# Optimization experiments

Hardware: AMD Instinct MI355X
Metric: run time of the kernel (lower is better)

## Reference

```python
import jax, jax.numpy as jnp
import numpy as np

NUM_HEADS = 16
EPS = 1e-5  # torch nn.LayerNorm default


def _ln(x, g, b):
    m = jnp.mean(x, axis=-1, keepdims=True)
    v = jnp.var(x, axis=-1, keepdims=True)
    return (x - m) / jnp.sqrt(v + EPS) * g + b


def _attn(q, k, v, proj_w, proj_b):
    B, N, C = q.shape
    S = k.shape[1]
    H = NUM_HEADS
    D = C // H
    qh = q.reshape(B, N, H, D).transpose(0, 2, 1, 3)
    kh = k.reshape(B, S, H, D).transpose(0, 2, 1, 3)
    vh = v.reshape(B, S, H, D).transpose(0, 2, 1, 3)
    scores = jnp.einsum('bhnd,bhsd->bhns', qh, kh) * (D ** -0.5)
    aw = jax.nn.softmax(scores, axis=-1)
    o = jnp.einsum('bhns,bhsd->bhnd', aw, vh)
    o = o.transpose(0, 2, 1, 3).reshape(B, N, C)
    return o @ proj_w + proj_b


def _mlp(x, w1, b1, w2, b2):
    h = jax.nn.gelu(x @ w1 + b1, approximate=False)  # torch nn.GELU (exact erf)
    return h @ w2 + b2


def setup_inputs() -> dict:
    key = jax.random.key(0)
    ks = jax.random.split(key, 12)
    B, N, C = 4, 512, 1024
    H = 4 * C
    s = 0.02
    return {
        'x': jax.random.normal(ks[0], (B, N, C), jnp.float32),
        'y': jax.random.normal(ks[1], (B, N, C), jnp.float32),
        'norm1_g': jnp.ones((C,), jnp.float32),
        'norm1_b': jnp.zeros((C,), jnp.float32),
        'norm2_g': jnp.ones((C,), jnp.float32),
        'norm2_b': jnp.zeros((C,), jnp.float32),
        'proj_w': jax.random.normal(ks[2], (C, C), jnp.float32) * s,
        'proj_b': jnp.zeros((C,), jnp.float32),
        'fc1_w': jax.random.normal(ks[3], (C, H), jnp.float32) * s,
        'fc1_b': jnp.zeros((H,), jnp.float32),
        'fc2_w': jax.random.normal(ks[4], (H, C), jnp.float32) * s,
        'fc2_b': jnp.zeros((C,), jnp.float32),
        'is_selfatt': 1,
    }


def reference(x, y, norm1_g, norm1_b, norm2_g, norm2_b, proj_w, proj_b,
              fc1_w, fc1_b, fc2_w, fc2_b, is_selfatt):
    for _ in range(4):
        if is_selfatt:
            xn = _ln(x, norm1_g, norm1_b)
            x = x + _attn(xn, xn, xn, proj_w, proj_b)
            x = x + _mlp(_ln(x, norm2_g, norm2_b), fc1_w, fc1_b, fc2_w, fc2_b)
            yn = _ln(y, norm1_g, norm1_b)
            y = y + _attn(yn, yn, yn, proj_w, proj_b)
            y = y + _mlp(_ln(y, norm2_g, norm2_b), fc1_w, fc1_b, fc2_w, fc2_b)
        xn = _ln(x, norm1_g, norm1_b)
        yn = _ln(y, norm1_g, norm1_b)
        x1 = x + _attn(xn, yn, yn, proj_w, proj_b)
        x1 = x1 + _mlp(_ln(x1, norm2_g, norm2_b), fc1_w, fc1_b, fc2_w, fc2_b)
        y1 = y + _attn(yn, xn, xn, proj_w, proj_b)
        y1 = y1 + _mlp(_ln(y1, norm2_g, norm2_b), fc1_w, fc1_b, fc2_w, fc2_b)
    return (x1, y1)
```

## Files before the change

kernel.cpp:

```cpp
#include <hip/hip_runtime.h>
#include <hip/hip_bf16.h>
#include <math.h>

#define BDIM 4
#define SEQ 512
#define CH 1024
#define NH 16
#define HD 64
#define HIDN 4096
#define ROWS (BDIM * SEQ)
#define MROWS (2 * ROWS)
#define BHTOT (BDIM * NH)

using bf16 = __hip_bfloat16;
typedef __attribute__((ext_vector_type(4))) float f32x4;
typedef __attribute__((ext_vector_type(8))) short bf16x8;

typedef __attribute__((address_space(1))) const unsigned int GU32;
typedef __attribute__((address_space(3))) unsigned int LU32;

__device__ __forceinline__ void gload16(const bf16* g, bf16* l) {
  __builtin_amdgcn_global_load_lds((GU32*)g, (LU32*)l, 16, 0, 0);
}

__global__ __launch_bounds__(256) void ln_bf16_kernel(
    const float* __restrict__ x, const float* __restrict__ g,
    const float* __restrict__ b, bf16* __restrict__ out) {
  int row = blockIdx.x;
  int t = threadIdx.x;
  const float4 v = reinterpret_cast<const float4*>(x + (size_t)row * CH)[t];
  float s = v.x + v.y + v.z + v.w;
  float s2 = v.x * v.x + v.y * v.y + v.z * v.z + v.w * v.w;
#pragma unroll
  for (int o = 32; o > 0; o >>= 1) {
    s += __shfl_down(s, o);
    s2 += __shfl_down(s2, o);
  }
  __shared__ float red[10];
  int lane = t & 63, wid = t >> 6;
  if (lane == 0) { red[wid] = s; red[4 + wid] = s2; }
  __syncthreads();
  if (t == 0) {
    float ts = red[0] + red[1] + red[2] + red[3];
    float ts2 = red[4] + red[5] + red[6] + red[7];
    float mean = ts * (1.0f / CH);
    float var = ts2 * (1.0f / CH) - mean * mean;
    red[8] = mean;
    red[9] = rsqrtf(var + 1e-5f);
  }
  __syncthreads();
  float mean = red[8], rstd = red[9];
  const float4 gv = reinterpret_cast<const float4*>(g)[t];
  const float4 bv = reinterpret_cast<const float4*>(b)[t];
  alignas(8) bf16 o4[4];
  o4[0] = __float2bfloat16((v.x - mean) * rstd * gv.x + bv.x);
  o4[1] = __float2bfloat16((v.y - mean) * rstd * gv.y + bv.y);
  o4[2] = __float2bfloat16((v.z - mean) * rstd * gv.z + bv.z);
  o4[3] = __float2bfloat16((v.w - mean) * rstd * gv.w + bv.w);
  reinterpret_cast<uint2*>(out + (size_t)row * CH)[t] = *reinterpret_cast<const uint2*>(o4);
}

__global__ __launch_bounds__(256) void head_transpose_kernel(
    const bf16* __restrict__ src, bf16* __restrict__ dst) {
  __shared__ bf16 t[32][33];
  int bh = blockIdx.z, b = bh >> 4, h = bh & 15;
  int s0 = blockIdx.x * 32, d0 = blockIdx.y * 32;
  int tx = threadIdx.x & 31, ty = threadIdx.x >> 5;
  const bf16* sp = src + ((size_t)(b * SEQ + s0)) * CH + h * HD + d0;
  for (int i = ty; i < 32; i += 8) t[i][tx] = sp[(size_t)i * CH + tx];
  __syncthreads();
  bf16* dp = dst + ((size_t)bh * HD + d0) * SEQ + s0;
  for (int i = ty; i < 32; i += 8) dp[(size_t)i * SEQ + tx] = t[tx][i];
}

__global__ __launch_bounds__(256) void wt_transpose_kernel(
    const float* __restrict__ W, bf16* __restrict__ WT, int K, int Nout) {
  __shared__ float t[32][33];
  int k0 = blockIdx.x * 32, n0 = blockIdx.y * 32;
  int tx = threadIdx.x & 31, ty = threadIdx.x >> 5;
  for (int i = ty; i < 32; i += 8)
    t[i][tx] = W[(size_t)(k0 + i) * Nout + n0 + tx];
  __syncthreads();
  for (int i = ty; i < 32; i += 8)
    WT[(size_t)(n0 + i) * K + k0 + tx] = __float2bfloat16(t[tx][i]);
}

template <int MODE>
__global__ __launch_bounds__(256) void gemm128(
    const bf16* __restrict__ A, int lda,
    const bf16* __restrict__ Bt, int ldb,
    void* __restrict__ Cout, int ldc,
    const float* __restrict__ base, const float* __restrict__ bias,
    int K) {
  int m0 = blockIdx.x * 128, n0 = blockIdx.y * 128;
  __shared__ bf16 As[3][128 * 32];
  __shared__ bf16 Bs[3][128 * 32];
  int tid = threadIdx.x, wid = tid >> 6, lane = tid & 63;
  int wr = wid >> 1, wc = wid & 1;
  int srow = tid >> 2;
  int scol = (tid & 3) << 3;
  const bf16* ga = &A[(size_t)(m0 + srow) * lda + scol];
  const bf16* gb = &Bt[(size_t)(n0 + srow) * ldb + scol];
  int fr = lane & 15, kr = lane >> 4;
  f32x4 acc[4][4] = {};

  auto stage = [&](int b, int k0) {
    gload16(ga + k0, As[b] + tid * 8);
    gload16(ga + (size_t)64 * lda + k0, As[b] + 2048 + tid * 8);
    gload16(gb + k0, Bs[b] + tid * 8);
    gload16(gb + (size_t)64 * ldb + k0, Bs[b] + 2048 + tid * 8);
  };
  auto compute = [&](int b) {
    bf16x8 aF[4], bF[4];
#pragma unroll
    for (int m = 0; m < 4; ++m)
      aF[m] = *reinterpret_cast<const bf16x8*>(&As[b][(wr * 64 + m * 16 + fr) * 32 + kr * 8]);
#pragma unroll
    for (int n = 0; n < 4; ++n)
      bF[n] = *reinterpret_cast<const bf16x8*>(&Bs[b][(wc * 64 + n * 16 + fr) * 32 + kr * 8]);
#pragma unroll
    for (int m = 0; m < 4; ++m)
#pragma unroll
      for (int n = 0; n < 4; ++n)
        acc[m][n] = __builtin_amdgcn_mfma_f32_16x16x32_bf16(aF[m], bF[n], acc[m][n], 0, 0, 0);
  };

  int nt = K / 32;
  stage(0, 0);
  stage(1, 32);
  for (int t = 0; t < nt - 2; ++t) {
    stage((t + 2) % 3, (t + 2) * 32);
    asm volatile("s_waitcnt vmcnt(8)" ::: "memory");
    __builtin_amdgcn_s_barrier();
    __builtin_amdgcn_sched_barrier(0);
    compute(t % 3);
    __builtin_amdgcn_s_barrier();
  }
  asm volatile("s_waitcnt vmcnt(4)" ::: "memory");
  __builtin_amdgcn_s_barrier();
  __builtin_amdgcn_sched_barrier(0);
  compute((nt - 2) % 3);
  asm volatile("s_waitcnt vmcnt(0)" ::: "memory");
  __builtin_amdgcn_s_barrier();
  __builtin_amdgcn_sched_barrier(0);
  compute((nt - 1) % 3);

  int colL = lane & 15;
  int rbase = (lane >> 4) * 4;
#pragma unroll
  for (int n = 0; n < 4; ++n) {
    int gc = n0 + wc * 64 + n * 16 + colL;
    float bv = bias ? bias[gc] : 0.0f;
#pragma unroll
    for (int m = 0; m < 4; ++m)
#pragma unroll
      for (int j = 0; j < 4; ++j) {
        int gr = m0 + wr * 64 + m * 16 + rbase + j;
        float v = acc[m][n][j] + bv;
        size_t idx = (size_t)gr * ldc + gc;
        if (MODE == 0) {
          ((float*)Cout)[idx] = base[idx] + v;
        } else {
          float gl = 0.5f * v * (1.0f + erff(v * 0.70710678118654752f));
          ((bf16*)Cout)[idx] = __float2bfloat16(gl);
        }
      }
  }
}

__global__ __launch_bounds__(512) void attn_fused(
    const bf16* __restrict__ ln1, const bf16* __restrict__ vT,
    bf16* __restrict__ out, int xorb) {
  __shared__ bf16 kv[3][64 * 64];
  __shared__ bf16 Pl[128 * 512];
  int bh = blockIdx.y;
  int b = bh >> 4, h = bh & 15;
  int kvb = b ^ xorb;
  int kvbh = kvb * NH + h;
  int m0 = blockIdx.x * 128;
  int tid = threadIdx.x, wid = tid >> 6, lane = tid & 63;
  int fr = lane & 15, kr = lane >> 4;
  int srow = tid >> 3;
  int scol8 = ((tid & 7) ^ (srow & 7)) << 3;
  const bf16* kbase = ln1 + ((size_t)(kvb * SEQ + srow)) * CH + h * HD + scol8;
  const bf16* vbase = vT + ((size_t)kvbh * HD + srow) * SEQ + scol8;

  int qrow = m0 + wid * 16 + fr;
  const bf16* qbase = ln1 + ((size_t)(b * SEQ) + qrow) * CH + h * HD;
  bf16x8 qF0 = *reinterpret_cast<const bf16x8*>(qbase + kr * 8);
  bf16x8 qF1 = *reinterpret_cast<const bf16x8*>(qbase + 32 + kr * 8);

  f32x4 acc[32];
#pragma unroll
  for (int n = 0; n < 32; ++n) acc[n] = (f32x4){0.f, 0.f, 0.f, 0.f};

  gload16(kbase, kv[0] + tid * 8);
  gload16(kbase + (size_t)64 * CH, kv[1] + tid * 8);
#pragma unroll
  for (int c = 0; c < 8; ++c) {
    if (c + 2 < 8) gload16(kbase + (size_t)(c + 2) * 64 * CH, kv[(c + 2) % 3] + tid * 8);
    if (c + 2 < 8)      asm volatile("s_waitcnt vmcnt(2)" ::: "memory");
    else if (c + 1 < 8) asm volatile("s_waitcnt vmcnt(1)" ::: "memory");
    else                asm volatile("s_waitcnt vmcnt(0)" ::: "memory");
    __builtin_amdgcn_s_barrier();
    __builtin_amdgcn_sched_barrier(0);
    const char* kb = (const char*)kv[c % 3];
#pragma unroll
    for (int nf = 0; nf < 4; ++nf) {
      int sl = nf * 16 + fr;
      int byt = sl * 128 + kr * 16;
      bf16x8 k0 = *reinterpret_cast<const bf16x8*>(kb + (byt ^ ((sl & 7) << 4)));
      bf16x8 k1 = *reinterpret_cast<const bf16x8*>(kb + ((byt + 64) ^ ((sl & 7) << 4)));
      acc[c * 4 + nf] = __builtin_amdgcn_mfma_f32_16x16x32_bf16(qF0, k0, acc[c * 4 + nf], 0, 0, 0);
      acc[c * 4 + nf] = __builtin_amdgcn_mfma_f32_16x16x32_bf16(qF1, k1, acc[c * 4 + nf], 0, 0, 0);
    }
    __builtin_amdgcn_s_barrier();
  }

  float mx[4], sum[4], inv[4];
#pragma unroll
  for (int j = 0; j < 4; ++j) {
    float m = acc[0][j];
#pragma unroll
    for (int n = 1; n < 32; ++n) m = fmaxf(m, acc[n][j]);
    m = fmaxf(m, __shfl_xor(m, 1));
    m = fmaxf(m, __shfl_xor(m, 2));
    m = fmaxf(m, __shfl_xor(m, 4));
    m = fmaxf(m, __shfl_xor(m, 8));
    mx[j] = m * 0.125f;
  }
#pragma unroll
  for (int j = 0; j < 4; ++j) sum[j] = 0.f;
#pragma unroll
  for (int n = 0; n < 32; ++n)
#pragma unroll
    for (int j = 0; j < 4; ++j) {
      float p = exp2f((acc[n][j] * 0.125f - mx[j]) * 1.4426950408889634f);
      acc[n][j] = p;
      sum[j] += p;
    }
#pragma unroll
  for (int j = 0; j < 4; ++j) {
    float s = sum[j];
    s += __shfl_xor(s, 1);
    s += __shfl_xor(s, 2);
    s += __shfl_xor(s, 4);
    s += __shfl_xor(s, 8);
    inv[j] = 1.0f / s;
  }
  {
    char* pb = (char*)Pl;
#pragma unroll
    for (int n = 0; n < 32; ++n)
#pragma unroll
      for (int j = 0; j < 4; ++j) {
        int pr = wid * 16 + (lane >> 4) * 4 + j;
        int pc = fr + 16 * n;
        int byt = (pr * 1024 + pc * 2) ^ ((pr & 7) << 4);
        *reinterpret_cast<bf16*>(pb + byt) = __float2bfloat16(acc[n][j]);
      }
  }

  f32x4 oacc[4] = {};
  int prow = wid * 16 + fr;
  gload16(vbase, kv[0] + tid * 8);
  gload16(vbase + 64, kv[1] + tid * 8);
#pragma unroll
  for (int c = 0; c < 8; ++c) {
    if (c + 2 < 8) gload16(vbase + (size_t)(c + 2) * 64, kv[(c + 2) % 3] + tid * 8);
    if (c + 2 < 8)      asm volatile("s_waitcnt vmcnt(2)" ::: "memory");
    else if (c + 1 < 8) asm volatile("s_waitcnt vmcnt(1)" ::: "memory");
    else                asm volatile("s_waitcnt vmcnt(0)" ::: "memory");
    __builtin_amdgcn_s_barrier();
    __builtin_amdgcn_sched_barrier(0);
    const char* vb = (const char*)kv[c % 3];
    const char* pb = (const char*)Pl;
#pragma unroll
    for (int ks = 0; ks < 2; ++ks) {
      int pby = (prow * 1024 + (c * 64 + ks * 32 + kr * 8) * 2) ^ ((prow & 7) << 4);
      bf16x8 pF = *reinterpret_cast<const bf16x8*>(pb + pby);
#pragma unroll
      for (int nf = 0; nf < 4; ++nf) {
        int dl = nf * 16 + fr;
        int vby = (dl * 128 + ks * 64 + kr * 16) ^ ((dl & 7) << 4);
        bf16x8 vF = *reinterpret_cast<const bf16x8*>(vb + vby);
        oacc[nf] = __builtin_amdgcn_mfma_f32_16x16x32_bf16(pF, vF, oacc[nf], 0, 0, 0);
      }
    }
    __builtin_amdgcn_s_barrier();
  }

#pragma unroll
  for (int nf = 0; nf < 4; ++nf)
#pragma unroll
    for (int j = 0; j < 4; ++j) {
      int r = m0 + wid * 16 + (lane >> 4) * 4 + j;
      int d = fr + 16 * nf;
      out[((size_t)(b * SEQ) + r) * CH + h * HD + d] = __float2bfloat16(oacc[nf][j] * inv[j]);
    }
}

extern "C" void kernel_launch(void* const* d_in, const int* in_sizes, int n_in,
                              void* d_out, int out_size, void* d_ws, size_t ws_size,
                              hipStream_t stream) {
  const float* x_in  = (const float*)d_in[0];
  const float* y_in  = (const float*)d_in[1];
  const float* n1g   = (const float*)d_in[2];
  const float* n1b   = (const float*)d_in[3];
  const float* n2g   = (const float*)d_in[4];
  const float* n2b   = (const float*)d_in[5];
  const float* projw = (const float*)d_in[6];
  const float* projb = (const float*)d_in[7];
  const float* fc1w  = (const float*)d_in[8];
  const float* fc1b  = (const float*)d_in[9];
  const float* fc2w  = (const float*)d_in[10];
  const float* fc2b  = (const float*)d_in[11];

  char* p = (char*)d_ws;
  auto alloc = [&](size_t bytes) {
    char* r = p;
    p += (bytes + 255) & ~(size_t)255;
    return r;
  };
  float* xybuf  = (float*)alloc((size_t)MROWS * CH * 4);
  float* x1y1   = (float*)alloc((size_t)MROWS * CH * 4);
  bf16*  ln1out = (bf16*)alloc((size_t)MROWS * CH * 2);
  bf16*  ln2out = (bf16*)alloc((size_t)MROWS * CH * 2);
  bf16*  vTall  = (bf16*)alloc((size_t)2 * BHTOT * HD * SEQ * 2);
  bf16*  attnout= (bf16*)alloc((size_t)MROWS * CH * 2);
  bf16*  hbuf   = (bf16*)alloc((size_t)MROWS * HIDN * 2);
  bf16*  projWT = (bf16*)alloc((size_t)CH * CH * 2);
  bf16*  fc1WT  = (bf16*)alloc((size_t)HIDN * CH * 2);
  bf16*  fc2WT  = (bf16*)alloc((size_t)CH * HIDN * 2);
  if ((size_t)(p - (char*)d_ws) > ws_size) return;

  float* outxy = (float*)d_out;

  hipMemcpyAsync(xybuf, x_in, (size_t)ROWS * CH * 4, hipMemcpyDeviceToDevice, stream);
  hipMemcpyAsync(xybuf + (size_t)ROWS * CH, y_in, (size_t)ROWS * CH * 4,
                 hipMemcpyDeviceToDevice, stream);

  wt_transpose_kernel<<<dim3(CH / 32, CH / 32), 256, 0, stream>>>(projw, projWT, CH, CH);
  wt_transpose_kernel<<<dim3(CH / 32, HIDN / 32), 256, 0, stream>>>(fc1w, fc1WT, CH, HIDN);
  wt_transpose_kernel<<<dim3(HIDN / 32, CH / 32), 256, 0, stream>>>(fc2w, fc2WT, HIDN, CH);

  auto attn_all = [&](int xorb) {
    attn_fused<<<dim3(SEQ / 128, 2 * BHTOT), 512, 0, stream>>>(ln1out, vTall, attnout, xorb);
  };
  auto proj_merged = [&](const float* rbase, float* dst) {
    gemm128<0><<<dim3(MROWS / 128, CH / 128), 256, 0, stream>>>(
        attnout, CH, projWT, CH, dst, CH, rbase, projb, CH);
  };
  auto mlp_merged = [&](const float* bsrc, float* dst) {
    ln_bf16_kernel<<<MROWS, 256, 0, stream>>>(bsrc, n2g, n2b, ln2out);
    gemm128<3><<<dim3(MROWS / 128, HIDN / 128), 256, 0, stream>>>(
        ln2out, CH, fc1WT, CH, hbuf, HIDN, nullptr, fc1b, CH);
    gemm128<0><<<dim3(MROWS / 128, CH / 128), 256, 0, stream>>>(
        hbuf, HIDN, fc2WT, HIDN, dst, CH, bsrc, fc2b, HIDN);
  };

  for (int it = 0; it < 4; ++it) {
    ln_bf16_kernel<<<MROWS, 256, 0, stream>>>(xybuf, n1g, n1b, ln1out);
    head_transpose_kernel<<<dim3(SEQ / 32, HD / 32, 2 * BHTOT), 256, 0, stream>>>(ln1out, vTall);
    attn_all(0);
    proj_merged(xybuf, xybuf);
    mlp_merged(xybuf, xybuf);
  }
  ln_bf16_kernel<<<MROWS, 256, 0, stream>>>(xybuf, n1g, n1b, ln1out);
  head_transpose_kernel<<<dim3(SEQ / 32, HD / 32, 2 * BHTOT), 256, 0, stream>>>(ln1out, vTall);
  attn_all(4);
  proj_merged(xybuf, x1y1);
  mlp_merged(x1y1, outxy);
}
```

Baseline: 1.169 ms.

## Swizzle GEMM LDS layout and parameterize pipeline ring depth

XOR-swizzles the 16-byte column chunks within each LDS row of the A/B tiles, so that MFMA fragment reads from different rows hit different banks. This aims to cut LDS bank conflicts. The software pipeline is generalized to a templated ring depth, with the N=1024 GEMMs using 4 stages to hide more global latency and fc1 keeping 3. The deeper ring uses more LDS per block, which may reduce occupancy, and the drain waitcnt logic is hand-coded per ring depth.

```diff
diff --git a/kernel.cpp b/kernel.cpp
--- a/kernel.cpp
+++ b/kernel.cpp
@@ -85,7 +85,7 @@
     WT[(size_t)(n0 + i) * K + k0 + tx] = __float2bfloat16(t[tx][i]);
 }
 
-template <int MODE>
+template <int MODE, int RING>
 __global__ __launch_bounds__(256) void gemm128(
     const bf16* __restrict__ A, int lda,
     const bf16* __restrict__ Bt, int ldb,
@@ -93,12 +93,12 @@
     const float* __restrict__ base, const float* __restrict__ bias,
     int K) {
   int m0 = blockIdx.x * 128, n0 = blockIdx.y * 128;
-  __shared__ bf16 As[3][128 * 32];
-  __shared__ bf16 Bs[3][128 * 32];
+  __shared__ bf16 As[RING][128 * 32];
+  __shared__ bf16 Bs[RING][128 * 32];
   int tid = threadIdx.x, wid = tid >> 6, lane = tid & 63;
   int wr = wid >> 1, wc = wid & 1;
   int srow = tid >> 2;
-  int scol = (tid & 3) << 3;
+  int scol = ((tid & 3) ^ (srow & 3)) << 3;
   const bf16* ga = &A[(size_t)(m0 + srow) * lda + scol];
   const bf16* gb = &Bt[(size_t)(n0 + srow) * ldb + scol];
   int fr = lane & 15, kr = lane >> 4;
@@ -113,11 +113,15 @@
   auto compute = [&](int b) {
     bf16x8 aF[4], bF[4];
 #pragma unroll
-    for (int m = 0; m < 4; ++m)
-      aF[m] = *reinterpret_cast<const bf16x8*>(&As[b][(wr * 64 + m * 16 + fr) * 32 + kr * 8]);
-#pragma unroll
-    for (int n = 0; n < 4; ++n)
-      bF[n] = *reinterpret_cast<const bf16x8*>(&Bs[b][(wc * 64 + n * 16 + fr) * 32 + kr * 8]);
+    for (int m = 0; m < 4; ++m) {
+      int R = wr * 64 + m * 16 + fr;
+      aF[m] = *reinterpret_cast<const bf16x8*>(&As[b][R * 32 + ((kr ^ (R & 3)) << 3)]);
+    }
+#pragma unroll
+    for (int n = 0; n < 4; ++n) {
+      int R = wc * 64 + n * 16 + fr;
+      bF[n] = *reinterpret_cast<const bf16x8*>(&Bs[b][R * 32 + ((kr ^ (R & 3)) << 3)]);
+    }
 #pragma unroll
     for (int m = 0; m < 4; ++m)
 #pragma unroll
@@ -126,24 +130,26 @@
   };
 
   int nt = K / 32;
-  stage(0, 0);
-  stage(1, 32);
-  for (int t = 0; t < nt - 2; ++t) {
-    stage((t + 2) % 3, (t + 2) * 32);
-    asm volatile("s_waitcnt vmcnt(8)" ::: "memory");
+#pragma unroll
+  for (int i = 0; i < RING - 1; ++i) stage(i, i * 32);
+  for (int t = 0; t < nt; ++t) {
+    int rem = nt - 1 - t;
+    if (rem >= RING - 1) {
+      stage((t + RING - 1) % RING, (t + RING - 1) * 32);
+      if (RING == 4) asm volatile("s_waitcnt vmcnt(12)" ::: "memory");
+      else           asm volatile("s_waitcnt vmcnt(8)" ::: "memory");
+    } else if (rem == 2) {
+      asm volatile("s_waitcnt vmcnt(8)" ::: "memory");
+    } else if (rem == 1) {
+      asm volatile("s_waitcnt vmcnt(4)" ::: "memory");
+    } else {
+      asm volatile("s_waitcnt vmcnt(0)" ::: "memory");
+    }
     __builtin_amdgcn_s_barrier();
     __builtin_amdgcn_sched_barrier(0);
-    compute(t % 3);
-    __builtin_amdgcn_s_barrier();
-  }
-  asm volatile("s_waitcnt vmcnt(4)" ::: "memory");
-  __builtin_amdgcn_s_barrier();
-  __builtin_amdgcn_sched_barrier(0);
-  compute((nt - 2) % 3);
-  asm volatile("s_waitcnt vmcnt(0)" ::: "memory");
-  __builtin_amdgcn_s_barrier();
-  __builtin_amdgcn_sched_barrier(0);
-  compute((nt - 1) % 3);
+    compute(t % RING);
+    __builtin_amdgcn_s_barrier();
+  }
 
   int colL = lane & 15;
   int rbase = (lane >> 4) * 4;
@@ -348,14 +354,14 @@
     attn_fused<<<dim3(SEQ / 128, 2 * BHTOT), 512, 0, stream>>>(ln1out, vTall, attnout, xorb);
   };
   auto proj_merged = [&](const float* rbase, float* dst) {
-    gemm128<0><<<dim3(MROWS / 128, CH / 128), 256, 0, stream>>>(
+    gemm128<0, 4><<<dim3(MROWS / 128, CH / 128), 256, 0, stream>>>(
         attnout, CH, projWT, CH, dst, CH, rbase, projb, CH);
   };
   auto mlp_merged = [&](const float* bsrc, float* dst) {
     ln_bf16_kernel<<<MROWS, 256, 0, stream>>>(bsrc, n2g, n2b, ln2out);
-    gemm128<3><<<dim3(MROWS / 128, HIDN / 128), 256, 0, stream>>>(
+    gemm128<3, 3><<<dim3(MROWS / 128, HIDN / 128), 256, 0, stream>>>(
         ln2out, CH, fc1WT, CH, hbuf, HIDN, nullptr, fc1b, CH);
-    gemm128<0><<<dim3(MROWS / 128, CH / 128), 256, 0, stream>>>(
+    gemm128<0, 4><<<dim3(MROWS / 128, CH / 128), 256, 0, stream>>>(
         hbuf, HIDN, fc2WT, HIDN, dst, CH, bsrc, fc2b, HIDN);
   };
 
```

New measurement: 1.194 ms. 1.02x slower.
